# Optimization experiments

Hardware: AMD Instinct MI355X
Metric: run time of the kernel (lower is better)

## Reference

```python
import jax, jax.numpy as jnp
import numpy as np

N = 100000   # nodes
E = 1600000  # directed edges
BN_EPS = 1e-5


def setup_inputs() -> dict:
    key = jax.random.key(0)
    ks = jax.random.split(key, 16)
    x = jax.random.normal(ks[0], (N, 24), dtype=jnp.float32)
    edge_index = jax.random.randint(ks[1], (2, E), 0, N, dtype=jnp.int32)

    def glorot(k, fan_in, fan_out):
        s = jnp.sqrt(6.0 / (fan_in + fan_out)).astype(jnp.float32)
        return jax.random.uniform(k, (fan_in, fan_out), jnp.float32, -s, s)

    return {
        "x": x, "edge_index": edge_index,
        "W1": glorot(ks[2], 24, 128),  "b1": jnp.zeros((128,), jnp.float32),
        "g1": jnp.ones((128,), jnp.float32), "be1": jnp.zeros((128,), jnp.float32),
        "W2": glorot(ks[3], 128, 128), "b2": jnp.zeros((128,), jnp.float32),
        "g2": jnp.ones((128,), jnp.float32), "be2": jnp.zeros((128,), jnp.float32),
        "W3": glorot(ks[4], 128, 64),  "b3": jnp.zeros((64,), jnp.float32),
        "g3": jnp.ones((64,), jnp.float32), "be3": jnp.zeros((64,), jnp.float32),
        "W4": glorot(ks[5], 64, 2),    "b4": jnp.zeros((2,), jnp.float32),
    }


def _gcn_norm(edge_index, n):
    # add self loops, compute D^{-1/2}(A+I)D^{-1/2} edge weights (PyG gcn_norm)
    loop = jnp.arange(n, dtype=edge_index.dtype)
    src = jnp.concatenate([edge_index[0], loop])
    dst = jnp.concatenate([edge_index[1], loop])
    deg = jax.ops.segment_sum(jnp.ones_like(src, dtype=jnp.float32), dst, num_segments=n)
    dinv = jnp.where(deg > 0, jax.lax.rsqrt(deg), 0.0)
    norm = dinv[src] * dinv[dst]  # [E+N]
    return src, dst, norm


def _gcn_conv(x, W, b, src, dst, norm, n):
    h = x @ W                                # [N, F_out] GEMM first (PyG order)
    msg = h[src] * norm[:, None]             # gather + edge scale
    agg = jax.ops.segment_sum(msg, dst, num_segments=n)  # scatter-add
    return agg + b


def _bn(x, gamma, beta):
    # BatchNorm1d, training-mode statistics (biased variance), dropout omitted (eval)
    mean = jnp.mean(x, axis=0)
    var = jnp.var(x, axis=0)
    return (x - mean) * jax.lax.rsqrt(var + BN_EPS) * gamma + beta


def reference(x, edge_index, W1, b1, g1, be1, W2, b2, g2, be2,
              W3, b3, g3, be3, W4, b4):
    n = x.shape[0]
    src, dst, norm = _gcn_norm(edge_index, n)
    h = _bn(jax.nn.relu(_gcn_conv(x, W1, b1, src, dst, norm, n)), g1, be1)
    h = _bn(jax.nn.relu(_gcn_conv(h, W2, b2, src, dst, norm, n)), g2, be2)
    h = _bn(jax.nn.relu(_gcn_conv(h, W3, b3, src, dst, norm, n)), g3, be3)
    out = _gcn_conv(h, W4, b4, src, dst, norm, n)
    return jax.nn.log_softmax(out, axis=1)
```

## Files before the change

### kernel.cpp

```cpp
#include <hip/hip_runtime.h>
#include <hip/hip_fp16.h>

#define BN_EPS 1e-5f

__global__ void k_zero_i(int* __restrict__ p, int n) {
    int i = blockIdx.x * blockDim.x + threadIdx.x;
    if (i < n) p[i] = 0;
}

__global__ void k_count(const int* __restrict__ dst, int* __restrict__ cnt, int E) {
    int e = blockIdx.x * blockDim.x + threadIdx.x;
    if (e < E) atomicAdd(&cnt[dst[e]], 1);
}

__global__ void k_dinv(const int* __restrict__ cnt, float* __restrict__ dinv, int n) {
    int i = blockIdx.x * blockDim.x + threadIdx.x;
    if (i < n) dinv[i] = rsqrtf((float)(cnt[i] + 1));
}

__global__ void k_scan1(const int* __restrict__ cnt, int* __restrict__ rs,
                        int* __restrict__ bsum, int n) {
    __shared__ int sh[1024];
    const int t = threadIdx.x;
    const int gid = blockIdx.x * 1024 + t;
    int v = (gid < n) ? cnt[gid] : 0;
    sh[t] = v;
    __syncthreads();
    for (int off = 1; off < 1024; off <<= 1) {
        int u = (t >= off) ? sh[t - off] : 0;
        __syncthreads();
        sh[t] += u;
        __syncthreads();
    }
    if (gid < n) rs[gid] = sh[t] - v;
    if (t == 1023) bsum[blockIdx.x] = sh[1023];
}

__global__ void k_scan2(int* __restrict__ bsum, int nb) {
    __shared__ int sh[1024];
    const int t = threadIdx.x;
    int v = (t < nb) ? bsum[t] : 0;
    sh[t] = v;
    __syncthreads();
    for (int off = 1; off < 1024; off <<= 1) {
        int u = (t >= off) ? sh[t - off] : 0;
        __syncthreads();
        sh[t] += u;
        __syncthreads();
    }
    if (t < nb) bsum[t] = sh[t] - v;
}

__global__ void k_scan3(int* __restrict__ rs, int* __restrict__ cur,
                        const int* __restrict__ bsum, int n) {
    int i = blockIdx.x * blockDim.x + threadIdx.x;
    if (i < n) {
        int v = rs[i] + bsum[i >> 10];
        rs[i] = v;
        cur[i] = v;
    }
}

__global__ void k_bcnt(const int* __restrict__ cnt, int* __restrict__ bcnt,
                       int n, int nb) {
    int b = blockIdx.x * blockDim.x + threadIdx.x;
    if (b >= nb) return;
    int s = 0;
    int base = b << 7;
    for (int k = 0; k < 128; ++k) {
        int id = base + k;
        if (id < n) s += cnt[id];
    }
    bcnt[b] = s;
}

__global__ void k_bscan(const int* __restrict__ bcnt, int* __restrict__ bcur, int nb) {
    __shared__ int sh[1024];
    const int t = threadIdx.x;
    int v = (t < nb) ? bcnt[t] : 0;
    sh[t] = v;
    __syncthreads();
    for (int off = 1; off < 1024; off <<= 1) {
        int u = (t >= off) ? sh[t - off] : 0;
        __syncthreads();
        sh[t] += u;
        __syncthreads();
    }
    if (t < nb) bcur[t * 32] = sh[t] - v;
}

__global__ void k_pass1(const int* __restrict__ src, const int* __restrict__ dst,
                        int* __restrict__ bcur, int2* __restrict__ pairs, int E) {
    int e = blockIdx.x * blockDim.x + threadIdx.x;
    if (e < E) {
        int d = dst[e];
        int pos = atomicAdd(&bcur[(d >> 7) * 32], 1);
        pairs[pos] = make_int2(d, src[e]);
    }
}

__global__ void k_pass2(const int2* __restrict__ pairs, int* __restrict__ cur,
                        int* __restrict__ csrc, int E) {
    int e = blockIdx.x * blockDim.x + threadIdx.x;
    if (e < E) {
        int2 p = pairs[e];
        int pos = atomicAdd(&cur[p.x], 1);
        csrc[pos] = p.y;
    }
}

__global__ void k_x2h(const float* __restrict__ x, __half* __restrict__ xh, int total4) {
    int i = blockIdx.x * blockDim.x + threadIdx.x;
    int idx = i * 4;
    if (idx < total4 * 4) {
        float4 v = *(const float4*)&x[idx];
        union { uint2 u; __half2 h[2]; } o;
        o.h[0] = __floats2half2_rn(v.x, v.y);
        o.h[1] = __floats2half2_rn(v.z, v.w);
        *(uint2*)&xh[idx] = o.u;
    }
}

__global__ void k_agg24h(const __half* __restrict__ xh, const int* __restrict__ rs,
                         const int* __restrict__ rend, const int* __restrict__ csrc,
                         const float* __restrict__ dinv, float* __restrict__ XA, int n) {
    const int g = threadIdx.x >> 3;
    const int j = threadIdx.x & 7;
    const bool act = (j < 6);
    union U { uint2 u; __half2 h[2]; };
    for (int d = blockIdx.x * 32 + g; d < n; d += gridDim.x * 32) {
        const float di = dinv[d];
        const int beg = rs[d], end = rend[d];
        float4 acc = make_float4(0.f, 0.f, 0.f, 0.f);
        if (act) {
            U u; u.u = *(const uint2*)&xh[(size_t)d * 24 + 4 * j];
            float2 f0 = __half22float2(u.h[0]), f1 = __half22float2(u.h[1]);
            acc.x = f0.x * di; acc.y = f0.y * di; acc.z = f1.x * di; acc.w = f1.y * di;
        }
        int e = beg;
        for (; e + 3 < end; e += 4) {
            int s0 = csrc[e], s1 = csrc[e + 1], s2 = csrc[e + 2], s3 = csrc[e + 3];
            float w0 = dinv[s0], w1 = dinv[s1], w2 = dinv[s2], w3 = dinv[s3];
            if (act) {
                U u0, u1, u2, u3;
                u0.u = *(const uint2*)&xh[(size_t)s0 * 24 + 4 * j];
                u1.u = *(const uint2*)&xh[(size_t)s1 * 24 + 4 * j];
                u2.u = *(const uint2*)&xh[(size_t)s2 * 24 + 4 * j];
                u3.u = *(const uint2*)&xh[(size_t)s3 * 24 + 4 * j];
                float2 a0 = __half22float2(u0.h[0]), b0 = __half22float2(u0.h[1]);
                float2 a1 = __half22float2(u1.h[0]), b1 = __half22float2(u1.h[1]);
                float2 a2 = __half22float2(u2.h[0]), b2 = __half22float2(u2.h[1]);
                float2 a3 = __half22float2(u3.h[0]), b3 = __half22float2(u3.h[1]);
                acc.x = fmaf(a0.x, w0, acc.x); acc.y = fmaf(a0.y, w0, acc.y);
                acc.z = fmaf(b0.x, w0, acc.z); acc.w = fmaf(b0.y, w0, acc.w);
                acc.x = fmaf(a1.x, w1, acc.x); acc.y = fmaf(a1.y, w1, acc.y);
                acc.z = fmaf(b1.x, w1, acc.z); acc.w = fmaf(b1.y, w1, acc.w);
                acc.x = fmaf(a2.x, w2, acc.x); acc.y = fmaf(a2.y, w2, acc.y);
                acc.z = fmaf(b2.x, w2, acc.z); acc.w = fmaf(b2.y, w2, acc.w);
                acc.x = fmaf(a3.x, w3, acc.x); acc.y = fmaf(a3.y, w3, acc.y);
                acc.z = fmaf(b3.x, w3, acc.z); acc.w = fmaf(b3.y, w3, acc.w);
            }
        }
        for (; e < end; ++e) {
            int s = csrc[e];
            float w = dinv[s];
            if (act) {
                U u; u.u = *(const uint2*)&xh[(size_t)s * 24 + 4 * j];
                float2 f0 = __half22float2(u.h[0]), f1 = __half22float2(u.h[1]);
                acc.x = fmaf(f0.x, w, acc.x); acc.y = fmaf(f0.y, w, acc.y);
                acc.z = fmaf(f1.x, w, acc.z); acc.w = fmaf(f1.y, w, acc.w);
            }
        }
        if (act) {
            acc.x *= di; acc.y *= di; acc.z *= di; acc.w *= di;
            *(float4*)&XA[(size_t)d * 24 + 4 * j] = acc;
        }
    }
}

template<int K, int F, int RT, bool AFF, bool EPI>
__global__ __launch_bounds__(256) void k_gemm2(const float* __restrict__ X,
        const float* __restrict__ W, const float* __restrict__ aff,
        void* __restrict__ Ov, const float* __restrict__ b,
        float* __restrict__ sums, int n) {
    constexpr int COLG = F / 4;
    constexpr int ROWG = 256 / COLG;
    constexpr int TR = ROWG * RT;
    __shared__ float sW[K * F];
    __shared__ float sX[TR * K];
    __shared__ float sRed[2 * F];
    const int tid = threadIdx.x;
    const int tx = tid % COLG;
    const int ty = tid / COLG;

    for (int i = tid * 4; i < K * F; i += 1024)
        *(float4*)&sW[i] = *(const float4*)&W[i];

    float4 bv;
    float ls[4], lq[4];
    if constexpr (EPI) {
        bv = *(const float4*)&b[tx * 4];
        #pragma unroll
        for (int c = 0; c < 4; ++c) { ls[c] = 0.f; lq[c] = 0.f; }
    }

    const int ntiles = (n + TR - 1) / TR;
    for (int tile = blockIdx.x; tile < ntiles; tile += gridDim.x) {
        const int r0 = tile * TR;
        __syncthreads();
        for (int i = tid * 4; i < TR * K; i += 1024) {
            const int row = i / K;
            const int kk = i % K;
            float4 v;
            if (r0 + row < n) {
                v = *(const float4*)&X[(size_t)(r0 + row) * K + kk];
                if constexpr (AFF) {
                    v.x = fmaf(v.x, aff[kk],     aff[K + kk]);
                    v.y = fmaf(v.y, aff[kk + 1], aff[K + kk + 1]);
                    v.z = fmaf(v.z, aff[kk + 2], aff[K + kk + 2]);
                    v.w = fmaf(v.w, aff[kk + 3], aff[K + kk + 3]);
                }
            } else {
                v = make_float4(0.f, 0.f, 0.f, 0.f);
            }
            *(float4*)&sX[i] = v;
        }
        __syncthreads();

        float acc[RT][4];
        #pragma unroll
        for (int r = 0; r < RT; ++r)
            #pragma unroll
            for (int c = 0; c < 4; ++c) acc[r][c] = 0.0f;

        for (int k4 = 0; k4 < K; k4 += 4) {
            float xk[RT][4];
            #pragma unroll
            for (int r = 0; r < RT; ++r) {
                float4 t = *(const float4*)&sX[(ty * RT + r) * K + k4];
                xk[r][0] = t.x; xk[r][1] = t.y; xk[r][2] = t.z; xk[r][3] = t.w;
            }
            float4 wv[4];
            #pragma unroll
            for (int kk = 0; kk < 4; ++kk)
                wv[kk] = *(const float4*)&sW[(k4 + kk) * F + tx * 4];
            #pragma unroll
            for (int kk = 0; kk < 4; ++kk)
                #pragma unroll
                for (int r = 0; r < RT; ++r) {
                    const float xr = xk[r][kk];
                    acc[r][0] = fmaf(xr, wv[kk].x, acc[r][0]);
                    acc[r][1] = fmaf(xr, wv[kk].y, acc[r][1]);
                    acc[r][2] = fmaf(xr, wv[kk].z, acc[r][2]);
                    acc[r][3] = fmaf(xr, wv[kk].w, acc[r][3]);
                }
        }

        #pragma unroll
        for (int r = 0; r < RT; ++r) {
            const int row = r0 + ty * RT + r;
            if (row < n) {
                if constexpr (EPI) {
                    float4 o;
                    o.x = fmaxf(acc[r][0] + bv.x, 0.f);
                    o.y = fmaxf(acc[r][1] + bv.y, 0.f);
                    o.z = fmaxf(acc[r][2] + bv.z, 0.f);
                    o.w = fmaxf(acc[r][3] + bv.w, 0.f);
                    ls[0] += o.x; lq[0] += o.x * o.x;
                    ls[1] += o.y; lq[1] += o.y * o.y;
                    ls[2] += o.z; lq[2] += o.z * o.z;
                    ls[3] += o.w; lq[3] += o.w * o.w;
                    *(float4*)&((float*)Ov)[(size_t)row * F + tx * 4] = o;
                } else {
                    union { float2 f2; __half2 h2[2]; } u;
                    u.h2[0] = __floats2half2_rn(acc[r][0], acc[r][1]);
                    u.h2[1] = __floats2half2_rn(acc[r][2], acc[r][3]);
                    *(float2*)&((__half*)Ov)[(size_t)row * F + tx * 4] = u.f2;
                }
            }
        }
    }

    if constexpr (EPI) {
        __syncthreads();
        if (tid < 2 * F) sRed[tid] = 0.f;
        __syncthreads();
        #pragma unroll
        for (int c = 0; c < 4; ++c) {
            atomicAdd(&sRed[tx * 4 + c], ls[c]);
            atomicAdd(&sRed[F + tx * 4 + c], lq[c]);
        }
        __syncthreads();
        if (tid < F) {
            atomicAdd(&sums[tid], sRed[tid]);
            atomicAdd(&sums[F + tid], sRed[F + tid]);
        }
    }
}

template<int F>
__global__ __launch_bounds__(256) void k_aggh(const __half2* __restrict__ H2,
        const int* __restrict__ rs, const int* __restrict__ rend,
        const int* __restrict__ csrc, const float* __restrict__ dinv,
        const float* __restrict__ b, float* __restrict__ A,
        float* __restrict__ sums, int n) {
    constexpr int LPN = F / 2;
    constexpr int NPW = 64 / LPN;
    __shared__ float sR[2 * F];
    const int tid = threadIdx.x;
    const int lane = tid & 63;
    const int wid = tid >> 6;
    const int sub = lane / LPN;
    const int fl = lane % LPN;
    const float2 bv = make_float2(b[2 * fl], b[2 * fl + 1]);
    const int gw = blockIdx.x * 4 + wid;
    const int nw = gridDim.x * 4;
    float ls0 = 0.f, lq0 = 0.f, ls1 = 0.f, lq1 = 0.f;

    for (int d = gw * NPW + sub; d < n; d += nw * NPW) {
        const int beg = rs[d], end = rend[d];
        const float di = dinv[d];
        float2 h = __half22float2(H2[(size_t)d * LPN + fl]);
        float ax = h.x * di, ay = h.y * di;
        int j = beg;
        for (; j + 7 < end; j += 8) {
            int s[8];
            #pragma unroll
            for (int k = 0; k < 8; ++k) s[k] = csrc[j + k];
            float w[8]; __half2 hv[8];
            #pragma unroll
            for (int k = 0; k < 8; ++k) {
                w[k] = dinv[s[k]];
                hv[k] = H2[(size_t)s[k] * LPN + fl];
            }
            #pragma unroll
            for (int k = 0; k < 8; ++k) {
                float2 f = __half22float2(hv[k]);
                ax = fmaf(f.x, w[k], ax);
                ay = fmaf(f.y, w[k], ay);
            }
        }
        for (; j + 3 < end; j += 4) {
            int s[4];
            #pragma unroll
            for (int k = 0; k < 4; ++k) s[k] = csrc[j + k];
            float w[4]; __half2 hv[4];
            #pragma unroll
            for (int k = 0; k < 4; ++k) {
                w[k] = dinv[s[k]];
                hv[k] = H2[(size_t)s[k] * LPN + fl];
            }
            #pragma unroll
            for (int k = 0; k < 4; ++k) {
                float2 f = __half22float2(hv[k]);
                ax = fmaf(f.x, w[k], ax);
                ay = fmaf(f.y, w[k], ay);
            }
        }
        for (; j < end; ++j) {
            int s = csrc[j];
            float w = dinv[s];
            float2 f = __half22float2(H2[(size_t)s * LPN + fl]);
            ax = fmaf(f.x, w, ax);
            ay = fmaf(f.y, w, ay);
        }
        float vx = fmaxf(fmaf(ax, di, bv.x), 0.f);
        float vy = fmaxf(fmaf(ay, di, bv.y), 0.f);
        *(float2*)&A[(size_t)d * F + 2 * fl] = make_float2(vx, vy);
        ls0 += vx; lq0 += vx * vx;
        ls1 += vy; lq1 += vy * vy;
    }

    if (tid < 2 * F) sR[tid] = 0.f;
    __syncthreads();
    atomicAdd(&sR[2 * fl], ls0);
    atomicAdd(&sR[2 * fl + 1], ls1);
    atomicAdd(&sR[F + 2 * fl], lq0);
    atomicAdd(&sR[F + 2 * fl + 1], lq1);
    __syncthreads();
    if (tid < 2 * F) atomicAdd(&sums[tid], sR[tid]);
}

__global__ void k_bnprep(const float* __restrict__ sums, const float* __restrict__ g,
                         const float* __restrict__ be, float* __restrict__ aff,
                         int F, float invn) {
    int f = threadIdx.x;
    if (f < F) {
        float mean = sums[f] * invn;
        float var = sums[F + f] * invn - mean * mean;
        float a = rsqrtf(var + BN_EPS) * g[f];
        aff[f] = a;
        aff[F + f] = be[f] - mean * a;
    }
}

__global__ void k_gemm4(const float* __restrict__ X, const float* __restrict__ W,
                        const float* __restrict__ aff, float* __restrict__ H, int n) {
    int i = blockIdx.x * blockDim.x + threadIdx.x;
    if (i >= n) return;
    float a0 = 0.0f, a1 = 0.0f;
    #pragma unroll 8
    for (int k = 0; k < 64; ++k) {
        float v = X[i * 64 + k] * aff[k] + aff[64 + k];
        a0 = fmaf(v, W[2 * k], a0);
        a1 = fmaf(v, W[2 * k + 1], a1);
    }
    H[2 * i] = a0;
    H[2 * i + 1] = a1;
}

__global__ void k_last(const float* __restrict__ H, const int* __restrict__ rs,
                       const int* __restrict__ rend, const int* __restrict__ csrc,
                       const float* __restrict__ dinv, const float* __restrict__ b,
                       float* __restrict__ out, int n) {
    int d = blockIdx.x * blockDim.x + threadIdx.x;
    if (d >= n) return;
    const float di = dinv[d];
    float a0 = H[2 * d] * di, a1 = H[2 * d + 1] * di;
    const int beg = rs[d], end = rend[d];
    for (int j = beg; j < end; ++j) {
        int s = csrc[j];
        float w = dinv[s];
        a0 = fmaf(H[2 * s], w, a0);
        a1 = fmaf(H[2 * s + 1], w, a1);
    }
    float v0 = fmaf(a0, di, b[0]);
    float v1 = fmaf(a1, di, b[1]);
    float m = fmaxf(v0, v1);
    float l = logf(expf(v0 - m) + expf(v1 - m)) + m;
    out[2 * d] = v0 - l;
    out[2 * d + 1] = v1 - l;
}

extern "C" void kernel_launch(void* const* d_in, const int* in_sizes, int n_in,
                              void* d_out, int out_size, void* d_ws, size_t ws_size,
                              hipStream_t stream) {
    const float* x   = (const float*)d_in[0];
    const int*   ei  = (const int*)d_in[1];
    const float* W1  = (const float*)d_in[2];
    const float* b1  = (const float*)d_in[3];
    const float* g1  = (const float*)d_in[4];
    const float* be1 = (const float*)d_in[5];
    const float* W2  = (const float*)d_in[6];
    const float* b2  = (const float*)d_in[7];
    const float* g2  = (const float*)d_in[8];
    const float* be2 = (const float*)d_in[9];
    const float* W3  = (const float*)d_in[10];
    const float* b3  = (const float*)d_in[11];
    const float* g3  = (const float*)d_in[12];
    const float* be3 = (const float*)d_in[13];
    const float* W4  = (const float*)d_in[14];
    const float* b4  = (const float*)d_in[15];
    float* out = (float*)d_out;

    const int N = in_sizes[0] / 24;
    const int E = in_sizes[1] / 2;
    const int* srcI = ei;
    const int* dstI = ei + E;
    const int NB = (N + 127) >> 7;

    int* cnt   = (int*)d_ws;
    int* rs    = cnt + N;
    int* cur   = rs + N;
    int* csrc  = cur + N;
    int* bsum  = csrc + E;
    int* bcnt  = bsum + 1024;
    int* bcur  = bcnt + 1024;
    float* dinv = (float*)(bcur + 1024 * 32);
    float* Hbase = dinv + N;
    float* A    = Hbase + (size_t)N * 128;
    float* S    = A + (size_t)N * 128;
    float* sums1 = S,        *aff1 = S + 256;
    float* sums2 = S + 512,  *aff2 = S + 768;
    float* sums3 = S + 1024, *aff3 = S + 1152;
    int2*   pairs = (int2*)Hbase;
    float*  XA    = Hbase;
    __half* Hh    = (__half*)Hbase;
    float*  LG    = Hbase;
    __half* xh    = (__half*)A;

    hipMemsetAsync(S, 0, 1280 * sizeof(float), stream);

    const int TB = 256;
    const int nb1024 = (N + 1023) / 1024;

    k_zero_i<<<(N + TB - 1) / TB, TB, 0, stream>>>(cnt, N);
    k_count<<<(E + TB - 1) / TB, TB, 0, stream>>>(dstI, cnt, E);
    k_dinv<<<(N + TB - 1) / TB, TB, 0, stream>>>(cnt, dinv, N);
    k_scan1<<<nb1024, 1024, 0, stream>>>(cnt, rs, bsum, N);
    k_scan2<<<1, 1024, 0, stream>>>(bsum, nb1024);
    k_scan3<<<(N + TB - 1) / TB, TB, 0, stream>>>(rs, cur, bsum, N);
    k_bcnt<<<(NB + TB - 1) / TB, TB, 0, stream>>>(cnt, bcnt, N, NB);
    k_bscan<<<1, 1024, 0, stream>>>(bcnt, bcur, NB);
    k_pass1<<<(E + TB - 1) / TB, TB, 0, stream>>>(srcI, dstI, bcur, pairs, E);
    k_pass2<<<(E + TB - 1) / TB, TB, 0, stream>>>(pairs, cur, csrc, E);

    k_x2h<<<(N * 24 / 4 + TB - 1) / TB, TB, 0, stream>>>(x, xh, N * 24 / 4);
    k_agg24h<<<2048, 256, 0, stream>>>(xh, rs, cur, csrc, dinv, XA, N);
    k_gemm2<24, 128, 4, false, true><<<1024, 256, 0, stream>>>(XA, W1, nullptr, A, b1, sums1, N);
    k_bnprep<<<1, 128, 0, stream>>>(sums1, g1, be1, aff1, 128, 1.0f / (float)N);

    k_gemm2<128, 128, 4, true, false><<<1024, 256, 0, stream>>>(A, W2, aff1, Hh, nullptr, nullptr, N);
    k_aggh<128><<<2048, 256, 0, stream>>>((const __half2*)Hh, rs, cur, csrc, dinv, b2, A, sums2, N);
    k_bnprep<<<1, 128, 0, stream>>>(sums2, g2, be2, aff2, 128, 1.0f / (float)N);

    k_gemm2<128, 64, 2, true, false><<<1024, 256, 0, stream>>>(A, W3, aff2, Hh, nullptr, nullptr, N);
    k_aggh<64><<<2048, 256, 0, stream>>>((const __half2*)Hh, rs, cur, csrc, dinv, b3, A, sums3, N);
    k_bnprep<<<1, 64, 0, stream>>>(sums3, g3, be3, aff3, 64, 1.0f / (float)N);

    k_gemm4<<<(N + TB - 1) / TB, TB, 0, stream>>>(A, W4, aff3, LG, N);
    k_last<<<(N + TB - 1) / TB, TB, 0, stream>>>(LG, rs, cur, csrc, dinv, b4, out, N);
}
```

Measured before the change: 680.6 us.

## Replace two-pass bucketed CSR fill with single XCD-partitioned fill kernel

Removes the block-count, block-scan and two-pass bucket sort used to build the CSR adjacency. Instead one kernel runs 8 block groups per edge chunk; each group only handles destinations whose (d>>7)&7 matches its slot. The intent is to keep atomics and csrc writes for a destination range local to one XCD's L2 and to skip the intermediate pairs buffer. The cost is that every edge's dst is read 8 times, and the XCD mapping assumes blocks are scheduled round-robin across XCDs by blockIdx.

After: 553.2 us. 18.7% less time.

```diff
diff --git a/kernel.cpp b/kernel.cpp
--- a/kernel.cpp
+++ b/kernel.cpp
@@ -61,51 +61,20 @@
     }
 }
 
-__global__ void k_bcnt(const int* __restrict__ cnt, int* __restrict__ bcnt,
-                       int n, int nb) {
-    int b = blockIdx.x * blockDim.x + threadIdx.x;
-    if (b >= nb) return;
-    int s = 0;
-    int base = b << 7;
-    for (int k = 0; k < 128; ++k) {
-        int id = base + k;
-        if (id < n) s += cnt[id];
-    }
-    bcnt[b] = s;
-}
-
-__global__ void k_bscan(const int* __restrict__ bcnt, int* __restrict__ bcur, int nb) {
-    __shared__ int sh[1024];
-    const int t = threadIdx.x;
-    int v = (t < nb) ? bcnt[t] : 0;
-    sh[t] = v;
-    __syncthreads();
-    for (int off = 1; off < 1024; off <<= 1) {
-        int u = (t >= off) ? sh[t - off] : 0;
-        __syncthreads();
-        sh[t] += u;
-        __syncthreads();
-    }
-    if (t < nb) bcur[t * 32] = sh[t] - v;
-}
-
-__global__ void k_pass1(const int* __restrict__ src, const int* __restrict__ dst,
-                        int* __restrict__ bcur, int2* __restrict__ pairs, int E) {
-    int e = blockIdx.x * blockDim.x + threadIdx.x;
-    if (e < E) {
+__global__ void k_fillx(const int* __restrict__ src, const int* __restrict__ dst,
+                        int* __restrict__ cur, int* __restrict__ csrc,
+                        int E, int nchunk) {
+    const int chunk = blockIdx.x >> 3;
+    const int myx = blockIdx.x & 7;
+    const int per = (E + nchunk - 1) / nchunk;
+    const int lo = chunk * per;
+    const int hi = min(lo + per, E);
+    for (int e = lo + threadIdx.x; e < hi; e += blockDim.x) {
         int d = dst[e];
-        int pos = atomicAdd(&bcur[(d >> 7) * 32], 1);
-        pairs[pos] = make_int2(d, src[e]);
-    }
-}
-
-__global__ void k_pass2(const int2* __restrict__ pairs, int* __restrict__ cur,
-                        int* __restrict__ csrc, int E) {
-    int e = blockIdx.x * blockDim.x + threadIdx.x;
-    if (e < E) {
-        int2 p = pairs[e];
-        int pos = atomicAdd(&cur[p.x], 1);
-        csrc[pos] = p.y;
+        if (((d >> 7) & 7) == myx) {
+            int pos = atomicAdd(&cur[d], 1);
+            csrc[pos] = src[e];
+        }
     }
 }
 
@@ -457,23 +426,19 @@
     const int E = in_sizes[1] / 2;
     const int* srcI = ei;
     const int* dstI = ei + E;
-    const int NB = (N + 127) >> 7;
 
     int* cnt   = (int*)d_ws;
     int* rs    = cnt + N;
     int* cur   = rs + N;
     int* csrc  = cur + N;
     int* bsum  = csrc + E;
-    int* bcnt  = bsum + 1024;
-    int* bcur  = bcnt + 1024;
-    float* dinv = (float*)(bcur + 1024 * 32);
+    float* dinv = (float*)(bsum + 1024);
     float* Hbase = dinv + N;
     float* A    = Hbase + (size_t)N * 128;
     float* S    = A + (size_t)N * 128;
     float* sums1 = S,        *aff1 = S + 256;
     float* sums2 = S + 512,  *aff2 = S + 768;
     float* sums3 = S + 1024, *aff3 = S + 1152;
-    int2*   pairs = (int2*)Hbase;
     float*  XA    = Hbase;
     __half* Hh    = (__half*)Hbase;
     float*  LG    = Hbase;
@@ -490,10 +455,7 @@
     k_scan1<<<nb1024, 1024, 0, stream>>>(cnt, rs, bsum, N);
     k_scan2<<<1, 1024, 0, stream>>>(bsum, nb1024);
     k_scan3<<<(N + TB - 1) / TB, TB, 0, stream>>>(rs, cur, bsum, N);
-    k_bcnt<<<(NB + TB - 1) / TB, TB, 0, stream>>>(cnt, bcnt, N, NB);
-    k_bscan<<<1, 1024, 0, stream>>>(bcnt, bcur, NB);
-    k_pass1<<<(E + TB - 1) / TB, TB, 0, stream>>>(srcI, dstI, bcur, pairs, E);
-    k_pass2<<<(E + TB - 1) / TB, TB, 0, stream>>>(pairs, cur, csrc, E);
+    k_fillx<<<256 * 8, TB, 0, stream>>>(srcI, dstI, cur, csrc, E, 256);
 
     k_x2h<<<(N * 24 / 4 + TB - 1) / TB, TB, 0, stream>>>(x, xh, N * 24 / 4);
     k_agg24h<<<2048, 256, 0, stream>>>(xh, rs, cur, csrc, dinv, XA, N);
```
